# Kernel optimization log

Measured on AMD Instinct MI355X. Metric: run time of the kernel, lower is better.

Reference implementation:

```python
import jax, jax.numpy as jnp
import numpy as np

N = 20000
E = 320000
IN_F = 128
HEADS = 8
OUT_F = 32
NEG_SLOPE = 0.2


def setup_inputs() -> dict:
    key = jax.random.key(0)
    k = jax.random.split(key, 8)
    x = jax.random.normal(k[0], (N, IN_F), dtype=jnp.float32)
    edge_index = jax.random.randint(k[1], (2, E), 0, N, dtype=jnp.int32)
    # Linear weights stored torch-style: [out, in]
    scale = 1.0 / np.sqrt(IN_F)
    W = jax.random.normal(k[2], (HEADS * OUT_F, IN_F), dtype=jnp.float32) * scale
    W1 = jax.random.normal(k[3], (HEADS * OUT_F, IN_F), dtype=jnp.float32) * scale
    W2 = jax.random.normal(k[4], (HEADS * OUT_F, IN_F), dtype=jnp.float32) * scale
    att = jax.random.normal(k[5], (1, HEADS, OUT_F), dtype=jnp.float32) * 0.1
    bias = jnp.zeros((HEADS * OUT_F,), dtype=jnp.float32)
    return {"x": x, "edge_index": edge_index, "W": W, "W1": W1, "W2": W2,
            "att": att, "bias": bias}


def reference(x, edge_index, W, W1, W2, att, bias):
    n, heads, out_f = x.shape[0], att.shape[1], att.shape[2]
    src, dst = edge_index[0], edge_index[1]

    # Node projections: [N, H, F]
    h_src = (x @ W1.T).reshape(n, heads, out_f)
    h_dst = (x @ W2.T).reshape(n, heads, out_f)
    values = (x @ W.T).reshape(n, heads, out_f)

    # Edge-wise GATv2 logits: a^T LeakyReLU(W1 h_i + W2 h_j)  -> [E, H]
    att_input = jax.nn.leaky_relu(h_src[src] + h_dst[dst], negative_slope=NEG_SLOPE)
    logits = jnp.einsum('ehf,hf->eh', att_input, att[0])

    # Segment softmax over incoming edges of each dst node (stable).
    seg_max = jax.ops.segment_max(logits, dst, num_segments=n)  # [N, H]
    exp_l = jnp.exp(logits - seg_max[dst])
    denom = jax.ops.segment_sum(exp_l, dst, num_segments=n)     # [N, H]
    weights = exp_l / denom[dst]                                # [E, H]

    # Weighted aggregation of source values into dst nodes.
    weighted = weights[:, :, None] * values[src]                # [E, H, F]
    out = jax.ops.segment_sum(weighted, dst, num_segments=n)    # [N, H, F]

    out = out.reshape(n, heads * out_f) + bias
    return out
```

## Files before the change

### kernel.cpp

```cpp
#include <hip/hip_runtime.h>
#include <math.h>

#define NN 20000
#define EE 320000
#define KF 128
#define HO 256
#define CAP 96

typedef __attribute__((ext_vector_type(8))) short short8;
typedef __attribute__((ext_vector_type(4))) float f32x4;
typedef __attribute__((ext_vector_type(2))) _Float16 half2_t;

static __device__ __forceinline__ unsigned short f2bf(float f) {
    union { float f; unsigned u; } v; v.f = f;
    unsigned u = v.u;
    u += 0x7fffu + ((u >> 16) & 1u);
    return (unsigned short)(u >> 16);
}
static __device__ __forceinline__ unsigned short f2h(float f) {
    _Float16 h = (_Float16)f;
    return __builtin_bit_cast(unsigned short, h);
}
static __device__ __forceinline__ float dot2f(half2_t a, half2_t b, float c) {
#if __has_builtin(__builtin_amdgcn_fdot2)
    return __builtin_amdgcn_fdot2(a, b, c, false);
#else
    return c + (float)a[0] * (float)b[0] + (float)a[1] * (float)b[1];
#endif
}

__global__ __launch_bounds__(256) void prep_kernel(
    const float* __restrict__ x, const float* __restrict__ W0,
    const float* __restrict__ W1, const float* __restrict__ W2,
    unsigned short* __restrict__ xb, unsigned short* __restrict__ wb,
    int* __restrict__ cursor)
{
    const int b = blockIdx.x;
    const int t = threadIdx.x;
    if (b < 96) {
        const int m = b >> 5;
        const float* __restrict__ Wm = (m == 0) ? W0 : (m == 1) ? W1 : W2;
        int idx = (b & 31) * 1024 + t * 4;
        float4 v = *(const float4*)(Wm + idx);
        ushort4 o;
        o.x = f2bf(v.x); o.y = f2bf(v.y); o.z = f2bf(v.z); o.w = f2bf(v.w);
        *(ushort4*)(wb + (size_t)m * 32768 + idx) = o;
    } else if (b < 2596) {
        size_t i = (size_t)(b - 96) * 1024 + t * 4;
        float4 v = *(const float4*)(x + i);
        ushort4 o;
        o.x = f2bf(v.x); o.y = f2bf(v.y); o.z = f2bf(v.z); o.w = f2bf(v.w);
        *(ushort4*)(xb + i) = o;
    } else {
        int i = (b - 2596) * 256 + t;
        if (i < NN) cursor[i] = 0;
    }
}

__global__ __launch_bounds__(256, 4) void mid_kernel(
    const unsigned short* __restrict__ xb, const unsigned short* __restrict__ wb,
    unsigned short* __restrict__ hv, unsigned short* __restrict__ hdst,
    const int* __restrict__ ei, int* __restrict__ cursor, int* __restrict__ csr_src)
{
    const int bid = blockIdx.x;
    if (bid < 1250) {
        const int e = bid * 256 + threadIdx.x;
        if (e < EE) {
            int s = ei[e];
            int d = ei[EE + e];
            int pos = atomicAdd(&cursor[d], 1);
            if (pos < CAP) csr_src[d * CAP + pos] = s;
        }
        return;
    }
    const int pb = bid - 1250;
    const int m  = (pb < 313) ? 0 : (pb < 626) ? 1 : 2;
    const int bx = pb - m * 313;
    const unsigned short* __restrict__ Wm = wb + (size_t)m * 32768;
    unsigned short* __restrict__ dst = (m == 0) ? (hv + 256) : (m == 1) ? hv : hdst;
    const int stride = (m == 2) ? 256 : 512;

    const int w    = threadIdx.x >> 6;
    const int lane = threadIdx.x & 63;
    const int lr   = lane & 15;
    const int q    = lane >> 4;
    const int cb   = w * 64;

    short8 Bf[4][4];
#pragma unroll
    for (int nt = 0; nt < 4; ++nt)
#pragma unroll
        for (int ks = 0; ks < 4; ++ks)
            Bf[nt][ks] = *(const short8*)(Wm + (size_t)(cb + nt * 16 + lr) * KF + ks * 32 + q * 8);

    const int rb = bx * 64;

#pragma unroll
    for (int it = 0; it < 4; ++it) {
        const int r0 = rb + it * 16;

        short8 Af[4];
        const int arow = r0 + lr;
#pragma unroll
        for (int ks = 0; ks < 4; ++ks) {
            Af[ks] = (short8){0,0,0,0,0,0,0,0};
            if (arow < NN)
                Af[ks] = *(const short8*)(xb + (size_t)arow * KF + ks * 32 + q * 8);
        }

        f32x4 acc[4];
#pragma unroll
        for (int nt = 0; nt < 4; ++nt) acc[nt] = (f32x4){0.f, 0.f, 0.f, 0.f};

#pragma unroll
        for (int ks = 0; ks < 4; ++ks)
#pragma unroll
            for (int nt = 0; nt < 4; ++nt)
                acc[nt] = __builtin_amdgcn_mfma_f32_16x16x32_bf16(Af[ks], Bf[nt][ks], acc[nt], 0, 0, 0);

#pragma unroll
        for (int nt = 0; nt < 4; ++nt) {
#pragma unroll
            for (int r = 0; r < 4; ++r) {
                const int row = r0 + q * 4 + r;
                if (row < NN) {
                    const float val = acc[nt][r];
                    dst[(size_t)row * stride + cb + nt * 16 + lr] =
                        (m == 0) ? f2bf(val) : f2h(val);
                }
            }
        }
    }
}

__global__ __launch_bounds__(128) void gat_kernel(
    const unsigned short* __restrict__ hv, const unsigned short* __restrict__ hdst,
    const float* __restrict__ att, const float* __restrict__ bias,
    const int* __restrict__ cursor, const int* __restrict__ csr_src,
    float* __restrict__ out)
{
    const int w    = threadIdx.x >> 6;
    const int d    = blockIdx.x * 2 + w;
    const int lane = threadIdx.x & 63;
    const int col  = lane * 4;

    const float4 av = *(const float4*)(att + col);
    const half2_t a6_01 = { (_Float16)(0.6f * av.x), (_Float16)(0.6f * av.y) };
    const half2_t a6_23 = { (_Float16)(0.6f * av.z), (_Float16)(0.6f * av.w) };
    const half2_t a4_01 = { (_Float16)(0.4f * av.x), (_Float16)(0.4f * av.y) };
    const half2_t a4_23 = { (_Float16)(0.4f * av.z), (_Float16)(0.4f * av.w) };
    const float4 b4 = *(const float4*)(bias + col);

    const uint2 hdb = *(const uint2*)(hdst + (size_t)d * HO + col);
    const half2_t hd01 = __builtin_bit_cast(half2_t, hdb.x);
    const half2_t hd23 = __builtin_bit_cast(half2_t, hdb.y);

    int deg = cursor[d];
    if (deg > CAP) deg = CAP;

    int sreg = (lane < deg) ? csr_src[d * CAP + lane] : 0;

    float l = 0.f;
    float o0 = 0.f, o1 = 0.f, o2 = 0.f, o3 = 0.f;

#define EDGE_CALC(HS, VV, VMUL)                                               \
    {                                                                         \
        half2_t z01 = __builtin_bit_cast(half2_t, HS.x) + hd01;               \
        half2_t z23 = __builtin_bit_cast(half2_t, HS.y) + hd23;               \
        unsigned zu01 = __builtin_bit_cast(unsigned, z01) & 0x7FFF7FFFu;      \
        unsigned zu23 = __builtin_bit_cast(unsigned, z23) & 0x7FFF7FFFu;      \
        float p = dot2f(a6_01, z01,                                           \
                  dot2f(a6_23, z23,                                           \
                  dot2f(a4_01, __builtin_bit_cast(half2_t, zu01),             \
                  dot2f(a4_23, __builtin_bit_cast(half2_t, zu23), 0.f))));    \
        p += __shfl_xor(p, 1); p += __shfl_xor(p, 2); p += __shfl_xor(p, 4);  \
        const float e = __expf(p) * (VMUL);                                   \
        l += e;                                                               \
        const float v0 = __builtin_bit_cast(float, VV.x << 16);              \
        const float v1 = __builtin_bit_cast(float, VV.x & 0xFFFF0000u);      \
        const float v2 = __builtin_bit_cast(float, VV.y << 16);              \
        const float v3 = __builtin_bit_cast(float, VV.y & 0xFFFF0000u);      \
        o0 = fmaf(e, v0, o0); o1 = fmaf(e, v1, o1);                           \
        o2 = fmaf(e, v2, o2); o3 = fmaf(e, v3, o3);                           \
    }

    const int ng = (deg < 64) ? deg : 64;
    for (int i = 0; i < ng; i += 4) {
        const int j1 = (i + 1 < ng) ? i + 1 : ng - 1;
        const int j2 = (i + 2 < ng) ? i + 2 : ng - 1;
        const int j3 = (i + 3 < ng) ? i + 3 : ng - 1;
        const float m1 = (i + 1 < ng) ? 1.f : 0.f;
        const float m2 = (i + 2 < ng) ? 1.f : 0.f;
        const float m3 = (i + 3 < ng) ? 1.f : 0.f;
        const int s0 = __shfl(sreg, i);
        const int s1 = __shfl(sreg, j1);
        const int s2 = __shfl(sreg, j2);
        const int s3 = __shfl(sreg, j3);
        const unsigned short* p0 = hv + (size_t)s0 * 512 + col;
        const unsigned short* p1 = hv + (size_t)s1 * 512 + col;
        const unsigned short* p2 = hv + (size_t)s2 * 512 + col;
        const unsigned short* p3 = hv + (size_t)s3 * 512 + col;
        const uint2 hs0 = *(const uint2*)p0;
        const uint2 vv0 = *(const uint2*)(p0 + 256);
        const uint2 hs1 = *(const uint2*)p1;
        const uint2 vv1 = *(const uint2*)(p1 + 256);
        const uint2 hs2 = *(const uint2*)p2;
        const uint2 vv2 = *(const uint2*)(p2 + 256);
        const uint2 hs3 = *(const uint2*)p3;
        const uint2 vv3 = *(const uint2*)(p3 + 256);
        EDGE_CALC(hs0, vv0, 1.f);
        EDGE_CALC(hs1, vv1, m1);
        EDGE_CALC(hs2, vv2, m2);
        EDGE_CALC(hs3, vv3, m3);
    }
    for (int j = 64; j < deg; ++j) {
        const int s0 = csr_src[d * CAP + j];
        const unsigned short* p0 = hv + (size_t)s0 * 512 + col;
        const uint2 hs0 = *(const uint2*)p0;
        const uint2 vv0 = *(const uint2*)(p0 + 256);
        EDGE_CALC(hs0, vv0, 1.f);
    }
#undef EDGE_CALC

    const float inv = (deg > 0) ? 1.f / l : 0.f;
    float4 res;
    res.x = fmaf(o0, inv, b4.x);
    res.y = fmaf(o1, inv, b4.y);
    res.z = fmaf(o2, inv, b4.z);
    res.w = fmaf(o3, inv, b4.w);
    *(float4*)(out + (size_t)d * HO + col) = res;
}

extern "C" void kernel_launch(void* const* d_in, const int* in_sizes, int n_in,
                              void* d_out, int out_size, void* d_ws, size_t ws_size,
                              hipStream_t stream) {
    const float* x    = (const float*)d_in[0];
    const int*   ei   = (const int*)d_in[1];
    const float* W0   = (const float*)d_in[2];
    const float* W1   = (const float*)d_in[3];
    const float* W2   = (const float*)d_in[4];
    const float* att  = (const float*)d_in[5];
    const float* bias = (const float*)d_in[6];
    float* out = (float*)d_out;

    char* p = (char*)d_ws;
    unsigned short* hv   = (unsigned short*)p; p += (size_t)NN * 512 * 2;
    unsigned short* hdst = (unsigned short*)p; p += (size_t)NN * HO * 2;
    unsigned short* xb   = (unsigned short*)p; p += (size_t)NN * KF * 2;
    unsigned short* wb   = (unsigned short*)p; p += (size_t)3 * 32768 * 2;
    int* cursor  = (int*)p; p += (size_t)NN * sizeof(int);
    int* csr_src = (int*)p; p += (size_t)NN * CAP * sizeof(int);

    prep_kernel<<<2675, 256, 0, stream>>>(x, W0, W1, W2, xb, wb, cursor);
    mid_kernel<<<2189, 256, 0, stream>>>(xb, wb, hv, hdst, ei, cursor, csr_src);
    gat_kernel<<<NN / 2, 128, 0, stream>>>(hv, hdst, att, bias, cursor, csr_src, out);
}
```

Before: 157.3 us.

## Interleave src and value rows for single 16-byte gathers, unroll edges by 8

The projection epilogue now writes h_src and values interleaved per 4-feature group into one row, and stores values as fp16 instead of bf16. The GAT kernel can then fetch both with one 16-byte load per edge instead of two 8-byte loads. The edge loop is unrolled by 8 to keep more gathers in flight, exp is replaced by exp2 with log2(e) folded into the attention weights, and blocks grow to 4 waves. The wider unroll raises register pressure, and fp16 values change the precision and range of the aggregated data.

```diff
diff --git a/kernel.cpp b/kernel.cpp
--- a/kernel.cpp
+++ b/kernel.cpp
@@ -77,8 +77,8 @@
     const int m  = (pb < 313) ? 0 : (pb < 626) ? 1 : 2;
     const int bx = pb - m * 313;
     const unsigned short* __restrict__ Wm = wb + (size_t)m * 32768;
-    unsigned short* __restrict__ dst = (m == 0) ? (hv + 256) : (m == 1) ? hv : hdst;
-    const int stride = (m == 2) ? 256 : 512;
+    unsigned short* __restrict__ dstp = (m == 2) ? hdst : hv;
+    const int voff = (m == 0) ? 4 : 0;
 
     const int w    = threadIdx.x >> 6;
     const int lane = threadIdx.x & 63;
@@ -120,35 +120,38 @@
 
 #pragma unroll
         for (int nt = 0; nt < 4; ++nt) {
+            const int f = cb + nt * 16 + lr;
 #pragma unroll
             for (int r = 0; r < 4; ++r) {
                 const int row = r0 + q * 4 + r;
                 if (row < NN) {
-                    const float val = acc[nt][r];
-                    dst[(size_t)row * stride + cb + nt * 16 + lr] =
-                        (m == 0) ? f2bf(val) : f2h(val);
+                    const unsigned short hval = f2h(acc[nt][r]);
+                    if (m == 2) dstp[(size_t)row * 256 + f] = hval;
+                    else        dstp[(size_t)row * 512 + ((f >> 2) << 3) + (f & 3) + voff] = hval;
                 }
             }
         }
     }
 }
 
-__global__ __launch_bounds__(128) void gat_kernel(
+__global__ __launch_bounds__(256) void gat_kernel(
     const unsigned short* __restrict__ hv, const unsigned short* __restrict__ hdst,
     const float* __restrict__ att, const float* __restrict__ bias,
     const int* __restrict__ cursor, const int* __restrict__ csr_src,
     float* __restrict__ out)
 {
     const int w    = threadIdx.x >> 6;
-    const int d    = blockIdx.x * 2 + w;
+    const int d    = blockIdx.x * 4 + w;
     const int lane = threadIdx.x & 63;
     const int col  = lane * 4;
 
     const float4 av = *(const float4*)(att + col);
-    const half2_t a6_01 = { (_Float16)(0.6f * av.x), (_Float16)(0.6f * av.y) };
-    const half2_t a6_23 = { (_Float16)(0.6f * av.z), (_Float16)(0.6f * av.w) };
-    const half2_t a4_01 = { (_Float16)(0.4f * av.x), (_Float16)(0.4f * av.y) };
-    const half2_t a4_23 = { (_Float16)(0.4f * av.z), (_Float16)(0.4f * av.w) };
+    const float LOG2E = 1.4426950408889634f;
+    const float s6 = 0.6f * LOG2E, s4 = 0.4f * LOG2E;
+    const half2_t a6_01 = { (_Float16)(s6 * av.x), (_Float16)(s6 * av.y) };
+    const half2_t a6_23 = { (_Float16)(s6 * av.z), (_Float16)(s6 * av.w) };
+    const half2_t a4_01 = { (_Float16)(s4 * av.x), (_Float16)(s4 * av.y) };
+    const half2_t a4_23 = { (_Float16)(s4 * av.z), (_Float16)(s4 * av.w) };
     const float4 b4 = *(const float4*)(bias + col);
 
     const uint2 hdb = *(const uint2*)(hdst + (size_t)d * HO + col);
@@ -163,10 +166,10 @@
     float l = 0.f;
     float o0 = 0.f, o1 = 0.f, o2 = 0.f, o3 = 0.f;
 
-#define EDGE_CALC(HS, VV, VMUL)                                               \
+#define EDGE_CALC(G, VMUL)                                                    \
     {                                                                         \
-        half2_t z01 = __builtin_bit_cast(half2_t, HS.x) + hd01;               \
-        half2_t z23 = __builtin_bit_cast(half2_t, HS.y) + hd23;               \
+        half2_t z01 = __builtin_bit_cast(half2_t, G.x) + hd01;                \
+        half2_t z23 = __builtin_bit_cast(half2_t, G.y) + hd23;                \
         unsigned zu01 = __builtin_bit_cast(unsigned, z01) & 0x7FFF7FFFu;      \
         unsigned zu23 = __builtin_bit_cast(unsigned, z23) & 0x7FFF7FFFu;      \
         float p = dot2f(a6_01, z01,                                           \
@@ -174,51 +177,39 @@
                   dot2f(a4_01, __builtin_bit_cast(half2_t, zu01),             \
                   dot2f(a4_23, __builtin_bit_cast(half2_t, zu23), 0.f))));    \
         p += __shfl_xor(p, 1); p += __shfl_xor(p, 2); p += __shfl_xor(p, 4);  \
-        const float e = __expf(p) * (VMUL);                                   \
+        const float e = __builtin_amdgcn_exp2f(p) * (VMUL);                   \
         l += e;                                                               \
-        const float v0 = __builtin_bit_cast(float, VV.x << 16);              \
-        const float v1 = __builtin_bit_cast(float, VV.x & 0xFFFF0000u);      \
-        const float v2 = __builtin_bit_cast(float, VV.y << 16);              \
-        const float v3 = __builtin_bit_cast(float, VV.y & 0xFFFF0000u);      \
-        o0 = fmaf(e, v0, o0); o1 = fmaf(e, v1, o1);                           \
-        o2 = fmaf(e, v2, o2); o3 = fmaf(e, v3, o3);                           \
+        const half2_t v01 = __builtin_bit_cast(half2_t, G.z);                 \
+        const half2_t v23 = __builtin_bit_cast(half2_t, G.w);                 \
+        o0 = fmaf((float)v01[0], e, o0);                                      \
+        o1 = fmaf((float)v01[1], e, o1);                                      \
+        o2 = fmaf((float)v23[0], e, o2);                                      \
+        o3 = fmaf((float)v23[1], e, o3);                                      \
     }
 
     const int ng = (deg < 64) ? deg : 64;
-    for (int i = 0; i < ng; i += 4) {
-        const int j1 = (i + 1 < ng) ? i + 1 : ng - 1;
-        const int j2 = (i + 2 < ng) ? i + 2 : ng - 1;
-        const int j3 = (i + 3 < ng) ? i + 3 : ng - 1;
-        const float m1 = (i + 1 < ng) ? 1.f : 0.f;
-        const float m2 = (i + 2 < ng) ? 1.f : 0.f;
-        const float m3 = (i + 3 < ng) ? 1.f : 0.f;
-        const int s0 = __shfl(sreg, i);
-        const int s1 = __shfl(sreg, j1);
-        const int s2 = __shfl(sreg, j2);
-        const int s3 = __shfl(sreg, j3);
-        const unsigned short* p0 = hv + (size_t)s0 * 512 + col;
-        const unsigned short* p1 = hv + (size_t)s1 * 512 + col;
-        const unsigned short* p2 = hv + (size_t)s2 * 512 + col;
-        const unsigned short* p3 = hv + (size_t)s3 * 512 + col;
-        const uint2 hs0 = *(const uint2*)p0;
-        const uint2 vv0 = *(const uint2*)(p0 + 256);
-        const uint2 hs1 = *(const uint2*)p1;
-        const uint2 vv1 = *(const uint2*)(p1 + 256);
-        const uint2 hs2 = *(const uint2*)p2;
-        const uint2 vv2 = *(const uint2*)(p2 + 256);
-        const uint2 hs3 = *(const uint2*)p3;
-        const uint2 vv3 = *(const uint2*)(p3 + 256);
-        EDGE_CALC(hs0, vv0, 1.f);
-        EDGE_CALC(hs1, vv1, m1);
-        EDGE_CALC(hs2, vv2, m2);
-        EDGE_CALC(hs3, vv3, m3);
+    for (int i = 0; i < ng; i += 8) {
+        int   jj[8];
+        float mm[8];
+#pragma unroll
+        for (int u = 0; u < 8; ++u) {
+            const int j = i + u;
+            jj[u] = (j < ng) ? j : (ng - 1);
+            mm[u] = (j < ng) ? 1.f : 0.f;
+        }
+        uint4 G[8];
+#pragma unroll
+        for (int u = 0; u < 8; ++u) {
+            const int s = __shfl(sreg, jj[u]);
+            G[u] = *(const uint4*)(hv + (size_t)s * 512 + lane * 8);
+        }
+#pragma unroll
+        for (int u = 0; u < 8; ++u) EDGE_CALC(G[u], mm[u]);
     }
     for (int j = 64; j < deg; ++j) {
         const int s0 = csr_src[d * CAP + j];
-        const unsigned short* p0 = hv + (size_t)s0 * 512 + col;
-        const uint2 hs0 = *(const uint2*)p0;
-        const uint2 vv0 = *(const uint2*)(p0 + 256);
-        EDGE_CALC(hs0, vv0, 1.f);
+        const uint4 g = *(const uint4*)(hv + (size_t)s0 * 512 + lane * 8);
+        EDGE_CALC(g, 1.f);
     }
 #undef EDGE_CALC
 
@@ -253,5 +244,5 @@
 
     prep_kernel<<<2675, 256, 0, stream>>>(x, W0, W1, W2, xb, wb, cursor);
     mid_kernel<<<2189, 256, 0, stream>>>(xb, wb, hv, hdst, ei, cursor, csr_src);
-    gat_kernel<<<NN / 2, 128, 0, stream>>>(hv, hdst, att, bias, cursor, csr_src, out);
-}
+    gat_kernel<<<NN / 4, 256, 0, stream>>>(hv, hdst, att, bias, cursor, csr_src, out);
+}
```

Measured after the change: 158.8 us. About the same (+0.9%).
